# Performance work log

Hardware: AMD Instinct MI355X
Metric: run time of the kernel (lower is better)

Reference implementation:

```python
import jax, jax.numpy as jnp
import numpy as np

NUM_LAYERS = 16
ALPHA = 1.0
EPS = 1e-20

def setup_inputs() -> dict:
    key = jax.random.key(0)
    k1, k2, k3, k4 = jax.random.split(key, 4)
    B, S, M, G = 8, 9, 8, 512
    M2 = M * M
    return {
        "dict_real": jax.random.normal(k1, (B, S, M2, G), dtype=jnp.float32),
        "dict_imag": jax.random.normal(k2, (B, S, M2, G), dtype=jnp.float32),
        "cov_real": jax.random.normal(k3, (B, S, M, M), dtype=jnp.float32),
        "cov_imag": jax.random.normal(k4, (B, S, M, M), dtype=jnp.float32),
    }

def reference(dict_real, dict_imag, cov_real, cov_imag):
    D = (dict_real + 1j * dict_imag).astype(jnp.complex64)   # (B,S,M2,G) dictionary_band
    C = (cov_real + 1j * cov_imag).astype(jnp.complex64)     # (B,S,M,M) covariance matrix
    B, S, M, _ = C.shape
    G = D.shape[-1]
    # covariance_vector = cov.transpose(2,3).reshape(B,S,M2,1)
    r = jnp.swapaxes(C, 2, 3).reshape(B, S, M * M, 1)
    Dh = jnp.conj(jnp.swapaxes(D, 2, 3))                     # (B,S,G,M2)
    DhD = jnp.matmul(Dh, D)                                  # (B,S,G,G) Hermitian PSD
    Dhr = jnp.matmul(Dh, r)                                  # (B,S,G,1)
    # initial spectrum: real part, L2-normalized over grid dim
    res = jnp.real(Dhr).astype(jnp.float32)
    res = res / (jnp.linalg.norm(res, axis=2, keepdims=True) + EPS)
    # gamma = 1 / max|eig(D^H D)|; Hermitian PSD so eigvalsh gives same max magnitude
    eig = jnp.linalg.eigvalsh(DhD)                           # (B,S,G) real
    gamma = 1.0 / jnp.max(jnp.abs(eig), axis=2, keepdims=True)        # (B,S,1)
    lam = 0.5 * jnp.max(jnp.abs(Dhr), axis=2, keepdims=True).reshape(B, S, 1)
    theta = (ALPHA * lam * gamma).reshape(B, S, 1, 1)
    g = gamma.reshape(B, S, 1, 1).astype(jnp.complex64)
    I = jnp.eye(G, dtype=jnp.complex64)
    Wt = I - g * DhD                                         # (B,S,G,G)
    Wer = g * Dhr                                            # We @ r, constant per layer

    def step(res_c, _):
        s = jnp.matmul(Wt, res_c.astype(jnp.complex64)) + Wer
        res_new = jax.nn.relu(jnp.abs(s) - theta)            # soft-shrinkage on magnitude
        return res_new, res_new

    res_final, res_all = jax.lax.scan(step, res, None, length=NUM_LAYERS)
    result_init_all = jnp.moveaxis(res_all, 0, 2)            # (B,S,L,G,1)

    def minmax_norm(x):
        lo = jnp.min(x, axis=2, keepdims=True)
        hi = jnp.max(x, axis=2, keepdims=True)
        return (x - lo) / (hi - lo + EPS)

    result_ave = minmax_norm(jnp.mean(res_final, axis=1, keepdims=True).astype(jnp.float32))
    result = minmax_norm(res_final)
    return (result, result_ave, result_init_all)
```

## Files before the change

### kernel.cpp

```cpp
#include <hip/hip_runtime.h>
#include <math.h>

#define N_SQ   7
#define INV_P  (1.0f / 256.0f)
#define EPS_F  1e-20f
#define PH     72
#define PQ     67

typedef _Float16 h2    __attribute__((ext_vector_type(2)));
typedef _Float16 f16x8 __attribute__((ext_vector_type(8)));
typedef float    f32x4 __attribute__((ext_vector_type(4)));

__device__ inline float cdot2(h2 a, h2 b, float c) {
#if __has_builtin(__builtin_amdgcn_fdot2)
    return __builtin_amdgcn_fdot2(a, b, c, false);
#else
    return c + (float)a.x * (float)b.x + (float)a.y * (float)b.y;
#endif
}
__device__ inline h2 bch2(unsigned int x) { return __builtin_bit_cast(h2, x); }
__device__ inline h2 bch2f(float x)       { return __builtin_bit_cast(h2, x); }
__device__ inline float bcf(h2 x)         { return __builtin_bit_cast(float, x); }


__global__ __launch_bounds__(512, 1) void ista_main_kernel(
    const float* __restrict__ Dre, const float* __restrict__ Dim,
    const float* __restrict__ Cre, const float* __restrict__ Cim,
    float* __restrict__ out, float* __restrict__ ws)
{
    const int bs = blockIdx.x;
    const int t  = threadIdx.x;
    const int wv = t >> 6;
    const int ln = t & 63;
    const int c16 = ln & 15;
    const int qd  = ln >> 4;
    const float* __restrict__ dre = Dre + (size_t)bs * 32768;
    const float* __restrict__ dim = Dim + (size_t)bs * 32768;

    __shared__ __align__(16) float uBuf[9216];
    _Float16* ShRe = (_Float16*)uBuf;
    _Float16* ShIm = (_Float16*)uBuf + 64 * PH;
    float*    Q1   = uBuf + 4608;
    float*    sUp  = uBuf;
    float*    sHu  = uBuf + 1024;
    _Float16* sResH = (_Float16*)(uBuf + 1152);
    __shared__ __align__(16) float s_r[128];
    __shared__ float s_red[16];
    __shared__ float s_scal[8];

    if (t < 64) {
        int i = t >> 3, j = t & 7;
        s_r[2 * t]     = Cre[bs * 64 + j * 8 + i];
        s_r[2 * t + 1] = Cim[bs * 64 + j * 8 + i];
    }
    __syncthreads();

    float dhr_re = 0.f, dhr_im = 0.f;
    h2 dV[64];
    #pragma unroll
    for (int m = 0; m < 64; ++m) {
        float ar = dre[m * 512 + t], ai = dim[m * 512 + t];
        dV[m] = h2{(_Float16)ar, (_Float16)ai};
        float rr = s_r[2 * m], ri = s_r[2 * m + 1];
        dhr_re += ar * rr + ai * ri;
        dhr_im += ar * ri - ai * rr;
    }
    {
        float sv = dhr_re * dhr_re;
        float mv = sqrtf(dhr_re * dhr_re + dhr_im * dhr_im);
        for (int off = 32; off; off >>= 1) {
            sv += __shfl_down(sv, off, 64);
            mv = fmaxf(mv, __shfl_down(mv, off, 64));
        }
        if (ln == 0) { s_red[wv] = sv; s_red[8 + wv] = mv; }
        __syncthreads();
        if (t == 0) {
            float ss = 0.f, mm = 0.f;
            for (int k = 0; k < 8; ++k) { ss += s_red[k]; mm = fmaxf(mm, s_red[8 + k]); }
            s_scal[7] = ss; s_scal[2] = mm;
        }
        __syncthreads();
    }
    float res_g = dhr_re / (sqrtf(s_scal[7]) + EPS_F);

    const int tau0 = 2 * wv, tau1 = 2 * wv + 1;
    const int I0 = tau0 >> 2, J0 = tau0 & 3;
    const int I1 = tau1 >> 2, J1 = tau1 & 3;

    auto epilogue = [&](f32x4 P0, f32x4 Qa0, f32x4 P1, f32x4 Qa1, bool first, bool last) {
        #pragma unroll
        for (int r = 0; r < 4; ++r) {
            Q1[(I0 * 16 + qd * 4 + r) * PQ + J0 * 16 + c16] = Qa0[r];
            Q1[(I1 * 16 + qd * 4 + r) * PQ + J1 * 16 + c16] = Qa1[r];
        }
        float dv = 0.f;
        if (I0 == J0) {
            #pragma unroll
            for (int r = 0; r < 4; ++r) if (qd * 4 + r == c16) dv = fmaxf(dv, fabsf(P0[r]));
        }
        if (I1 == J1) {
            #pragma unroll
            for (int r = 0; r < 4; ++r) if (qd * 4 + r == c16) dv = fmaxf(dv, fabsf(P1[r]));
        }
        for (int off = 32; off; off >>= 1) dv = fmaxf(dv, __shfl_down(dv, off, 64));
        if (ln == 0) s_red[wv] = dv;
        __syncthreads();
        if (t == 0) {
            float m = 0.f;
            for (int k = 0; k < 8; ++k) m = fmaxf(m, s_red[k]);
            s_scal[3] = first ? logf(m) : 2.f * s_scal[3] + logf(m);
            s_scal[4] = 1.f / m;
        }
        __syncthreads();
        float ic = s_scal[4];
        float ci0[4], ci1[4];
        #pragma unroll
        for (int r = 0; r < 4; ++r) {
            ci0[r] = Qa0[r] - Q1[(J0 * 16 + c16) * PQ + I0 * 16 + qd * 4 + r];
            ci1[r] = Qa1[r] - Q1[(J1 * 16 + c16) * PQ + I1 * 16 + qd * 4 + r];
        }
        if (!last) {
            #pragma unroll
            for (int r = 0; r < 4; ++r) {
                ShRe[(I0 * 16 + qd * 4 + r) * PH + J0 * 16 + c16] = (_Float16)(P0[r] * ic);
                ShIm[(I0 * 16 + qd * 4 + r) * PH + J0 * 16 + c16] = (_Float16)(ci0[r] * ic);
                ShRe[(I1 * 16 + qd * 4 + r) * PH + J1 * 16 + c16] = (_Float16)(P1[r] * ic);
                ShIm[(I1 * 16 + qd * 4 + r) * PH + J1 * 16 + c16] = (_Float16)(ci1[r] * ic);
            }
            __syncthreads();
        } else {
            float fr = 0.f;
            #pragma unroll
            for (int r = 0; r < 4; ++r)
                fr += P0[r] * P0[r] + ci0[r] * ci0[r] + P1[r] * P1[r] + ci1[r] * ci1[r];
            fr *= ic * ic;
            for (int off = 32; off; off >>= 1) fr += __shfl_down(fr, off, 64);
            if (ln == 0) s_red[wv] = fr;
            __syncthreads();
            if (t == 0) {
                float fsum = 0.f;
                for (int k = 0; k < 8; ++k) fsum += s_red[k];
                float loglam = (2.f * s_scal[3] + logf(fsum)) * INV_P;
                float gamma = expf(-loglam);
                s_scal[0] = gamma;
                s_scal[1] = 0.5f * s_scal[2] * gamma;
            }
            __syncthreads();
        }
    };

    h2 du_re[32], du_im[32];
    f32x4 gP0 = {0.f, 0.f, 0.f, 0.f}, gQ0 = {0.f, 0.f, 0.f, 0.f};
    f32x4 gP1 = {0.f, 0.f, 0.f, 0.f}, gQ1 = {0.f, 0.f, 0.f, 0.f};
    {
        const int srow = t >> 4;
        const int scb  = (t & 15) * 4;
        float4 pr0, pi0, pr1, pi1;
        pr0 = *(const float4*)&dre[srow * 512 + scb];
        pi0 = *(const float4*)&dim[srow * 512 + scb];
        pr1 = *(const float4*)&dre[(srow + 32) * 512 + scb];
        pi1 = *(const float4*)&dim[(srow + 32) * 512 + scb];
        for (int ch = 0; ch < 8; ++ch) {
            *(h2*)&ShRe[srow * PH + scb]     = h2{(_Float16)pr0.x, (_Float16)pr0.y};
            *(h2*)&ShRe[srow * PH + scb + 2] = h2{(_Float16)pr0.z, (_Float16)pr0.w};
            *(h2*)&ShIm[srow * PH + scb]     = h2{(_Float16)pi0.x, (_Float16)pi0.y};
            *(h2*)&ShIm[srow * PH + scb + 2] = h2{(_Float16)pi0.z, (_Float16)pi0.w};
            *(h2*)&ShRe[(srow + 32) * PH + scb]     = h2{(_Float16)pr1.x, (_Float16)pr1.y};
            *(h2*)&ShRe[(srow + 32) * PH + scb + 2] = h2{(_Float16)pr1.z, (_Float16)pr1.w};
            *(h2*)&ShIm[(srow + 32) * PH + scb]     = h2{(_Float16)pi1.x, (_Float16)pi1.y};
            *(h2*)&ShIm[(srow + 32) * PH + scb + 2] = h2{(_Float16)pi1.z, (_Float16)pi1.w};
            if (ch < 7) {
                int gc = (ch + 1) * 64;
                pr0 = *(const float4*)&dre[srow * 512 + gc + scb];
                pi0 = *(const float4*)&dim[srow * 512 + gc + scb];
                pr1 = *(const float4*)&dre[(srow + 32) * 512 + gc + scb];
                pi1 = *(const float4*)&dim[(srow + 32) * 512 + gc + scb];
            }
            __syncthreads();
            #pragma unroll
            for (int ks = 0; ks < 64; ks += 32) {
                f16x8 arI0 = *(const f16x8*)&ShRe[(I0 * 16 + c16) * PH + ks + qd * 8];
                f16x8 aiI0 = *(const f16x8*)&ShIm[(I0 * 16 + c16) * PH + ks + qd * 8];
                f16x8 arJ0 = *(const f16x8*)&ShRe[(J0 * 16 + c16) * PH + ks + qd * 8];
                f16x8 aiJ0 = *(const f16x8*)&ShIm[(J0 * 16 + c16) * PH + ks + qd * 8];
                gP0 = __builtin_amdgcn_mfma_f32_16x16x32_f16(arI0, arJ0, gP0, 0, 0, 0);
                gP0 = __builtin_amdgcn_mfma_f32_16x16x32_f16(aiI0, aiJ0, gP0, 0, 0, 0);
                gQ0 = __builtin_amdgcn_mfma_f32_16x16x32_f16(aiI0, arJ0, gQ0, 0, 0, 0);
                f16x8 arI1 = *(const f16x8*)&ShRe[(I1 * 16 + c16) * PH + ks + qd * 8];
                f16x8 aiI1 = *(const f16x8*)&ShIm[(I1 * 16 + c16) * PH + ks + qd * 8];
                f16x8 arJ1 = *(const f16x8*)&ShRe[(J1 * 16 + c16) * PH + ks + qd * 8];
                f16x8 aiJ1 = *(const f16x8*)&ShIm[(J1 * 16 + c16) * PH + ks + qd * 8];
                gP1 = __builtin_amdgcn_mfma_f32_16x16x32_f16(arI1, arJ1, gP1, 0, 0, 0);
                gP1 = __builtin_amdgcn_mfma_f32_16x16x32_f16(aiI1, aiJ1, gP1, 0, 0, 0);
                gQ1 = __builtin_amdgcn_mfma_f32_16x16x32_f16(aiI1, arJ1, gQ1, 0, 0, 0);
            }
            if (ch == wv) {
                #pragma unroll
                for (int c = 0; c < 8; ++c) {
                    uint4 aw = *(const uint4*)&ShRe[ln * PH + 8 * c];
                    du_re[4 * c + 0] = bch2(aw.x); du_re[4 * c + 1] = bch2(aw.y);
                    du_re[4 * c + 2] = bch2(aw.z); du_re[4 * c + 3] = bch2(aw.w);
                    uint4 bw = *(const uint4*)&ShIm[ln * PH + 8 * c];
                    du_im[4 * c + 0] = bch2(bw.x); du_im[4 * c + 1] = bch2(bw.y);
                    du_im[4 * c + 2] = bch2(bw.z); du_im[4 * c + 3] = bch2(bw.w);
                }
            }
            __syncthreads();
        }
    }
    epilogue(gP0, gQ0, gP1, gQ1, true, false);

    for (int sq = 0; sq < N_SQ; ++sq) {
        f32x4 P0 = {0.f, 0.f, 0.f, 0.f}, Qa0 = {0.f, 0.f, 0.f, 0.f};
        f32x4 P1 = {0.f, 0.f, 0.f, 0.f}, Qa1 = {0.f, 0.f, 0.f, 0.f};
        #pragma unroll
        for (int ks = 0; ks < 64; ks += 32) {
            f16x8 arI0 = *(const f16x8*)&ShRe[(I0 * 16 + c16) * PH + ks + qd * 8];
            f16x8 aiI0 = *(const f16x8*)&ShIm[(I0 * 16 + c16) * PH + ks + qd * 8];
            f16x8 arJ0 = *(const f16x8*)&ShRe[(J0 * 16 + c16) * PH + ks + qd * 8];
            f16x8 aiJ0 = *(const f16x8*)&ShIm[(J0 * 16 + c16) * PH + ks + qd * 8];
            P0  = __builtin_amdgcn_mfma_f32_16x16x32_f16(arI0, arJ0, P0, 0, 0, 0);
            P0  = __builtin_amdgcn_mfma_f32_16x16x32_f16(aiI0, aiJ0, P0, 0, 0, 0);
            Qa0 = __builtin_amdgcn_mfma_f32_16x16x32_f16(aiI0, arJ0, Qa0, 0, 0, 0);
            f16x8 arI1 = *(const f16x8*)&ShRe[(I1 * 16 + c16) * PH + ks + qd * 8];
            f16x8 aiI1 = *(const f16x8*)&ShIm[(I1 * 16 + c16) * PH + ks + qd * 8];
            f16x8 arJ1 = *(const f16x8*)&ShRe[(J1 * 16 + c16) * PH + ks + qd * 8];
            f16x8 aiJ1 = *(const f16x8*)&ShIm[(J1 * 16 + c16) * PH + ks + qd * 8];
            P1  = __builtin_amdgcn_mfma_f32_16x16x32_f16(arI1, arJ1, P1, 0, 0, 0);
            P1  = __builtin_amdgcn_mfma_f32_16x16x32_f16(aiI1, aiJ1, P1, 0, 0, 0);
            Qa1 = __builtin_amdgcn_mfma_f32_16x16x32_f16(aiI1, arJ1, Qa1, 0, 0, 0);
        }
        epilogue(P0, Qa0, P1, Qa1, false, sq == N_SQ - 1);
    }

    const float gamma = s_scal[0];
    const float theta = s_scal[1];
    float* out_init = out + 40960 + (size_t)bs * 8192;
    const int resh_base = 64 * wv;

    for (int l = 0; l < 16; ++l) {
        sResH[t] = (_Float16)res_g;
        float upR = 0.f, upI = 0.f;
        #pragma unroll
        for (int c = 0; c < 8; ++c) {
            uint4 rw = *(const uint4*)&sResH[resh_base + 8 * c];
            h2 r0 = bch2(rw.x), r1 = bch2(rw.y), r2 = bch2(rw.z), r3 = bch2(rw.w);
            upR = cdot2(du_re[4 * c + 0], r0, upR);  upI = cdot2(du_im[4 * c + 0], r0, upI);
            upR = cdot2(du_re[4 * c + 1], r1, upR);  upI = cdot2(du_im[4 * c + 1], r1, upI);
            upR = cdot2(du_re[4 * c + 2], r2, upR);  upI = cdot2(du_im[4 * c + 2], r2, upI);
            upR = cdot2(du_re[4 * c + 3], r3, upR);  upI = cdot2(du_im[4 * c + 3], r3, upI);
        }
        *(float2*)&sUp[(wv * 64 + ln) * 2] = make_float2(upR, upI);
        __syncthreads();
        if (wv == 0) {
            float ufR = 0.f, ufI = 0.f;
            #pragma unroll
            for (int w8 = 0; w8 < 8; ++w8) {
                float2 p = *(const float2*)&sUp[(w8 * 64 + ln) * 2];
                ufR += p.x; ufI += p.y;
            }
            h2 hu1 = h2{(_Float16)ufR, (_Float16)ufI};
            h2 hu2 = h2{(_Float16)ufI, (_Float16)(-ufR)};
            *(float2*)&sHu[2 * ln] = make_float2(bcf(hu1), bcf(hu2));
        }
        __syncthreads();
        float wR = 0.f, wI = 0.f;
        #pragma unroll
        for (int mm = 0; mm < 32; ++mm) {
            float4 hq = *(const float4*)&sHu[4 * mm];
            wR = cdot2(dV[2 * mm],     bch2f(hq.x), wR);
            wI = cdot2(dV[2 * mm],     bch2f(hq.y), wI);
            wR = cdot2(dV[2 * mm + 1], bch2f(hq.z), wR);
            wI = cdot2(dV[2 * mm + 1], bch2f(hq.w), wI);
        }
        float sre = res_g + gamma * (dhr_re - wR);
        float sim = gamma * (dhr_im - wI);
        float mag = sqrtf(sre * sre + sim * sim);
        res_g = fmaxf(mag - theta, 0.f);
        out_init[l * 512 + t] = res_g;
    }

    {
        float mn = res_g, mx = res_g;
        for (int off = 32; off; off >>= 1) {
            mn = fminf(mn, __shfl_down(mn, off, 64));
            mx = fmaxf(mx, __shfl_down(mx, off, 64));
        }
        if (ln == 0) { s_red[wv] = mn; s_red[8 + wv] = mx; }
        __syncthreads();
        if (t == 0) {
            float a = s_red[0], b2 = s_red[8];
            for (int k = 1; k < 8; ++k) { a = fminf(a, s_red[k]); b2 = fmaxf(b2, s_red[8 + k]); }
            s_scal[5] = a; s_scal[6] = b2;
        }
        __syncthreads();
        out[bs * 512 + t] = (res_g - s_scal[5]) / (s_scal[6] - s_scal[5] + EPS_F);
        ws[bs * 512 + t] = res_g;
    }
}

__global__ __launch_bounds__(512) void ista_ave_kernel(
    const float* __restrict__ ws, float* __restrict__ out)
{
    const int b = blockIdx.x;
    const int g = threadIdx.x;
    __shared__ float s_red[16];
    __shared__ float s_scal[2];
    float acc = 0.f;
    #pragma unroll
    for (int s = 0; s < 9; ++s) acc += ws[(b * 9 + s) * 512 + g];
    acc *= (1.f / 9.f);
    float mn = acc, mx = acc;
    for (int off = 32; off; off >>= 1) {
        mn = fminf(mn, __shfl_down(mn, off, 64));
        mx = fmaxf(mx, __shfl_down(mx, off, 64));
    }
    if ((g & 63) == 0) { s_red[g >> 6] = mn; s_red[8 + (g >> 6)] = mx; }
    __syncthreads();
    if (g == 0) {
        float a = s_red[0], b2 = s_red[8];
        for (int k = 1; k < 8; ++k) { a = fminf(a, s_red[k]); b2 = fmaxf(b2, s_red[8 + k]); }
        s_scal[0] = a; s_scal[1] = b2;
    }
    __syncthreads();
    out[36864 + b * 512 + g] = (acc - s_scal[0]) / (s_scal[1] - s_scal[0] + EPS_F);
}

extern "C" void kernel_launch(void* const* d_in, const int* in_sizes, int n_in,
                              void* d_out, int out_size, void* d_ws, size_t ws_size,
                              hipStream_t stream) {
    const float* Dre = (const float*)d_in[0];
    const float* Dim = (const float*)d_in[1];
    const float* Cre = (const float*)d_in[2];
    const float* Cim = (const float*)d_in[3];
    float* out = (float*)d_out;
    float* ws  = (float*)d_ws;

    ista_main_kernel<<<72, 512, 0, stream>>>(Dre, Dim, Cre, Cim, out, ws);
    ista_ave_kernel<<<8, 512, 0, stream>>>(ws, out);
}
```

Before: 112.6 us.

## Double-buffer Gram staging, replace thread-0 reductions with redundant all-thread reductions, shuffle-broadcast updates

The Gram-matrix staging loop now alternates between two LDS buffers, which drops one barrier per chunk, and it folds the dictionary register loads and the D^H r accumulation into that same loop. Scalar reductions that thread 0 used to do through shared memory are now done redundantly by every thread, removing extra barriers. In the ISTA layers, the separate wave-0 reduction and its second barrier are replaced by every wave reducing the partial sums and broadcasting them with wave shuffles. Dual accumulators shorten the dependency chains, and launch bounds are raised to two blocks per CU, which may force register spills given the large per-thread register arrays.

```diff
diff --git a/kernel.cpp b/kernel.cpp
--- a/kernel.cpp
+++ b/kernel.cpp
@@ -23,7 +23,7 @@
 __device__ inline float bcf(h2 x)         { return __builtin_bit_cast(float, x); }
 
 
-__global__ __launch_bounds__(512, 1) void ista_main_kernel(
+__global__ __launch_bounds__(512, 2) void ista_main_kernel(
     const float* __restrict__ Dre, const float* __restrict__ Dim,
     const float* __restrict__ Cre, const float* __restrict__ Cim,
     float* __restrict__ out, float* __restrict__ ws)
@@ -38,33 +38,161 @@
     const float* __restrict__ dim = Dim + (size_t)bs * 32768;
 
     __shared__ __align__(16) float uBuf[9216];
-    _Float16* ShRe = (_Float16*)uBuf;
-    _Float16* ShIm = (_Float16*)uBuf + 64 * PH;
-    float*    Q1   = uBuf + 4608;
-    float*    sUp  = uBuf;
-    float*    sHu  = uBuf + 1024;
-    _Float16* sResH = (_Float16*)(uBuf + 1152);
+    _Float16* ShRe  = (_Float16*)uBuf;
+    _Float16* ShIm  = (_Float16*)uBuf + 64 * PH;
+    _Float16* ShReB = (_Float16*)uBuf + 2 * 64 * PH;
+    _Float16* ShImB = (_Float16*)uBuf + 3 * 64 * PH;
+    float*    Q1    = uBuf + 4608;
+    _Float16* sResH = (_Float16*)(uBuf + 2048);
     __shared__ __align__(16) float s_r[128];
     __shared__ float s_red[16];
-    __shared__ float s_scal[8];
 
     if (t < 64) {
         int i = t >> 3, j = t & 7;
         s_r[2 * t]     = Cre[bs * 64 + j * 8 + i];
         s_r[2 * t + 1] = Cim[bs * 64 + j * 8 + i];
     }
-    __syncthreads();
-
-    float dhr_re = 0.f, dhr_im = 0.f;
+
+    const int tau0 = 2 * wv, tau1 = 2 * wv + 1;
+    const int I0 = tau0 >> 2, J0 = tau0 & 3;
+    const int I1 = tau1 >> 2, J1 = tau1 & 3;
+
+    float Elog = 0.f, gamma = 0.f, theta = 0.f, mm = 0.f;
+
+    auto epilogue = [&](f32x4 P0, f32x4 Qa0, f32x4 P1, f32x4 Qa1, bool first, bool last) {
+        #pragma unroll
+        for (int r = 0; r < 4; ++r) {
+            Q1[(I0 * 16 + qd * 4 + r) * PQ + J0 * 16 + c16] = Qa0[r];
+            Q1[(I1 * 16 + qd * 4 + r) * PQ + J1 * 16 + c16] = Qa1[r];
+        }
+        float dv = 0.f;
+        if (I0 == J0) {
+            #pragma unroll
+            for (int r = 0; r < 4; ++r) if (qd * 4 + r == c16) dv = fmaxf(dv, fabsf(P0[r]));
+        }
+        if (I1 == J1) {
+            #pragma unroll
+            for (int r = 0; r < 4; ++r) if (qd * 4 + r == c16) dv = fmaxf(dv, fabsf(P1[r]));
+        }
+        for (int off = 32; off; off >>= 1) dv = fmaxf(dv, __shfl_down(dv, off, 64));
+        if (ln == 0) s_red[wv] = dv;
+        __syncthreads();
+        float m = s_red[0];
+        #pragma unroll
+        for (int k = 1; k < 8; ++k) m = fmaxf(m, s_red[k]);
+        Elog = first ? logf(m) : 2.f * Elog + logf(m);
+        float ic = 1.f / m;
+        float ci0[4], ci1[4];
+        #pragma unroll
+        for (int r = 0; r < 4; ++r) {
+            ci0[r] = Qa0[r] - Q1[(J0 * 16 + c16) * PQ + I0 * 16 + qd * 4 + r];
+            ci1[r] = Qa1[r] - Q1[(J1 * 16 + c16) * PQ + I1 * 16 + qd * 4 + r];
+        }
+        if (!last) {
+            #pragma unroll
+            for (int r = 0; r < 4; ++r) {
+                ShRe[(I0 * 16 + qd * 4 + r) * PH + J0 * 16 + c16] = (_Float16)(P0[r] * ic);
+                ShIm[(I0 * 16 + qd * 4 + r) * PH + J0 * 16 + c16] = (_Float16)(ci0[r] * ic);
+                ShRe[(I1 * 16 + qd * 4 + r) * PH + J1 * 16 + c16] = (_Float16)(P1[r] * ic);
+                ShIm[(I1 * 16 + qd * 4 + r) * PH + J1 * 16 + c16] = (_Float16)(ci1[r] * ic);
+            }
+            __syncthreads();
+        } else {
+            float fr = 0.f;
+            #pragma unroll
+            for (int r = 0; r < 4; ++r)
+                fr += P0[r] * P0[r] + ci0[r] * ci0[r] + P1[r] * P1[r] + ci1[r] * ci1[r];
+            fr *= ic * ic;
+            for (int off = 32; off; off >>= 1) fr += __shfl_down(fr, off, 64);
+            if (ln == 0) s_red[8 + wv] = fr;
+            __syncthreads();
+            float fsum = 0.f;
+            #pragma unroll
+            for (int k = 0; k < 8; ++k) fsum += s_red[8 + k];
+            float loglam = (2.f * Elog + logf(fsum)) * INV_P;
+            gamma = expf(-loglam);
+            theta = 0.5f * mm * gamma;
+        }
+    };
+
     h2 dV[64];
-    #pragma unroll
-    for (int m = 0; m < 64; ++m) {
-        float ar = dre[m * 512 + t], ai = dim[m * 512 + t];
-        dV[m] = h2{(_Float16)ar, (_Float16)ai};
-        float rr = s_r[2 * m], ri = s_r[2 * m + 1];
-        dhr_re += ar * rr + ai * ri;
-        dhr_im += ar * ri - ai * rr;
-    }
+    h2 du_re[32], du_im[32];
+    float dr0 = 0.f, dr1 = 0.f, di0 = 0.f, di1 = 0.f;
+    f32x4 gP0 = {0.f,0.f,0.f,0.f}, gQ0 = {0.f,0.f,0.f,0.f};
+    f32x4 gP1 = {0.f,0.f,0.f,0.f}, gQ1 = {0.f,0.f,0.f,0.f};
+    {
+        const int srow = t >> 4;
+        const int scb  = (t & 15) * 4;
+        float4 pr0 = *(const float4*)&dre[srow * 512 + scb];
+        float4 pi0 = *(const float4*)&dim[srow * 512 + scb];
+        float4 pr1 = *(const float4*)&dre[(srow + 32) * 512 + scb];
+        float4 pi1 = *(const float4*)&dim[(srow + 32) * 512 + scb];
+        #pragma unroll
+        for (int ch = 0; ch < 8; ++ch) {
+            _Float16* SRe = (ch & 1) ? ShReB : ShRe;
+            _Float16* SIm = (ch & 1) ? ShImB : ShIm;
+            *(h2*)&SRe[srow * PH + scb]       = h2{(_Float16)pr0.x, (_Float16)pr0.y};
+            *(h2*)&SRe[srow * PH + scb + 2]   = h2{(_Float16)pr0.z, (_Float16)pr0.w};
+            *(h2*)&SIm[srow * PH + scb]       = h2{(_Float16)pi0.x, (_Float16)pi0.y};
+            *(h2*)&SIm[srow * PH + scb + 2]   = h2{(_Float16)pi0.z, (_Float16)pi0.w};
+            *(h2*)&SRe[(srow + 32) * PH + scb]     = h2{(_Float16)pr1.x, (_Float16)pr1.y};
+            *(h2*)&SRe[(srow + 32) * PH + scb + 2] = h2{(_Float16)pr1.z, (_Float16)pr1.w};
+            *(h2*)&SIm[(srow + 32) * PH + scb]     = h2{(_Float16)pi1.x, (_Float16)pi1.y};
+            *(h2*)&SIm[(srow + 32) * PH + scb + 2] = h2{(_Float16)pi1.z, (_Float16)pi1.w};
+            if (ch < 7) {
+                int gc = (ch + 1) * 64;
+                pr0 = *(const float4*)&dre[srow * 512 + gc + scb];
+                pi0 = *(const float4*)&dim[srow * 512 + gc + scb];
+                pr1 = *(const float4*)&dre[(srow + 32) * 512 + gc + scb];
+                pi1 = *(const float4*)&dim[(srow + 32) * 512 + gc + scb];
+            }
+            float cr[8], cim8[8];
+            #pragma unroll
+            for (int k = 0; k < 8; ++k) {
+                cr[k]   = dre[(ch * 8 + k) * 512 + t];
+                cim8[k] = dim[(ch * 8 + k) * 512 + t];
+            }
+            __syncthreads();
+            #pragma unroll
+            for (int ks = 0; ks < 64; ks += 32) {
+                f16x8 arI0 = *(const f16x8*)&SRe[(I0 * 16 + c16) * PH + ks + qd * 8];
+                f16x8 aiI0 = *(const f16x8*)&SIm[(I0 * 16 + c16) * PH + ks + qd * 8];
+                f16x8 arJ0 = *(const f16x8*)&SRe[(J0 * 16 + c16) * PH + ks + qd * 8];
+                f16x8 aiJ0 = *(const f16x8*)&SIm[(J0 * 16 + c16) * PH + ks + qd * 8];
+                gP0 = __builtin_amdgcn_mfma_f32_16x16x32_f16(arI0, arJ0, gP0, 0, 0, 0);
+                gP0 = __builtin_amdgcn_mfma_f32_16x16x32_f16(aiI0, aiJ0, gP0, 0, 0, 0);
+                gQ0 = __builtin_amdgcn_mfma_f32_16x16x32_f16(aiI0, arJ0, gQ0, 0, 0, 0);
+                f16x8 arI1 = *(const f16x8*)&SRe[(I1 * 16 + c16) * PH + ks + qd * 8];
+                f16x8 aiI1 = *(const f16x8*)&SIm[(I1 * 16 + c16) * PH + ks + qd * 8];
+                f16x8 arJ1 = *(const f16x8*)&SRe[(J1 * 16 + c16) * PH + ks + qd * 8];
+                f16x8 aiJ1 = *(const f16x8*)&SIm[(J1 * 16 + c16) * PH + ks + qd * 8];
+                gP1 = __builtin_amdgcn_mfma_f32_16x16x32_f16(arI1, arJ1, gP1, 0, 0, 0);
+                gP1 = __builtin_amdgcn_mfma_f32_16x16x32_f16(aiI1, aiJ1, gP1, 0, 0, 0);
+                gQ1 = __builtin_amdgcn_mfma_f32_16x16x32_f16(aiI1, arJ1, gQ1, 0, 0, 0);
+            }
+            if (ch == wv) {
+                #pragma unroll
+                for (int c = 0; c < 8; ++c) {
+                    uint4 aw = *(const uint4*)&SRe[ln * PH + 8 * c];
+                    du_re[4 * c + 0] = bch2(aw.x); du_re[4 * c + 1] = bch2(aw.y);
+                    du_re[4 * c + 2] = bch2(aw.z); du_re[4 * c + 3] = bch2(aw.w);
+                    uint4 bw = *(const uint4*)&SIm[ln * PH + 8 * c];
+                    du_im[4 * c + 0] = bch2(bw.x); du_im[4 * c + 1] = bch2(bw.y);
+                    du_im[4 * c + 2] = bch2(bw.z); du_im[4 * c + 3] = bch2(bw.w);
+                }
+            }
+            #pragma unroll
+            for (int k = 0; k < 8; ++k) {
+                float ar = cr[k], ai = cim8[k];
+                dV[ch * 8 + k] = h2{(_Float16)ar, (_Float16)ai};
+                float rr = s_r[2 * (ch * 8 + k)], ri = s_r[2 * (ch * 8 + k) + 1];
+                if (k & 1) { dr1 += ar * rr + ai * ri; di1 += ar * ri - ai * rr; }
+                else       { dr0 += ar * rr + ai * ri; di0 += ar * ri - ai * rr; }
+            }
+        }
+    }
+    const float dhr_re = dr0 + dr1, dhr_im = di0 + di1;
+    float res_g;
     {
         float sv = dhr_re * dhr_re;
         float mv = sqrtf(dhr_re * dhr_re + dhr_im * dhr_im);
@@ -74,145 +202,18 @@
         }
         if (ln == 0) { s_red[wv] = sv; s_red[8 + wv] = mv; }
         __syncthreads();
-        if (t == 0) {
-            float ss = 0.f, mm = 0.f;
-            for (int k = 0; k < 8; ++k) { ss += s_red[k]; mm = fmaxf(mm, s_red[8 + k]); }
-            s_scal[7] = ss; s_scal[2] = mm;
-        }
-        __syncthreads();
-    }
-    float res_g = dhr_re / (sqrtf(s_scal[7]) + EPS_F);
-
-    const int tau0 = 2 * wv, tau1 = 2 * wv + 1;
-    const int I0 = tau0 >> 2, J0 = tau0 & 3;
-    const int I1 = tau1 >> 2, J1 = tau1 & 3;
-
-    auto epilogue = [&](f32x4 P0, f32x4 Qa0, f32x4 P1, f32x4 Qa1, bool first, bool last) {
-        #pragma unroll
-        for (int r = 0; r < 4; ++r) {
-            Q1[(I0 * 16 + qd * 4 + r) * PQ + J0 * 16 + c16] = Qa0[r];
-            Q1[(I1 * 16 + qd * 4 + r) * PQ + J1 * 16 + c16] = Qa1[r];
-        }
-        float dv = 0.f;
-        if (I0 == J0) {
-            #pragma unroll
-            for (int r = 0; r < 4; ++r) if (qd * 4 + r == c16) dv = fmaxf(dv, fabsf(P0[r]));
-        }
-        if (I1 == J1) {
-            #pragma unroll
-            for (int r = 0; r < 4; ++r) if (qd * 4 + r == c16) dv = fmaxf(dv, fabsf(P1[r]));
-        }
-        for (int off = 32; off; off >>= 1) dv = fmaxf(dv, __shfl_down(dv, off, 64));
-        if (ln == 0) s_red[wv] = dv;
-        __syncthreads();
-        if (t == 0) {
-            float m = 0.f;
-            for (int k = 0; k < 8; ++k) m = fmaxf(m, s_red[k]);
-            s_scal[3] = first ? logf(m) : 2.f * s_scal[3] + logf(m);
-            s_scal[4] = 1.f / m;
-        }
-        __syncthreads();
-        float ic = s_scal[4];
-        float ci0[4], ci1[4];
-        #pragma unroll
-        for (int r = 0; r < 4; ++r) {
-            ci0[r] = Qa0[r] - Q1[(J0 * 16 + c16) * PQ + I0 * 16 + qd * 4 + r];
-            ci1[r] = Qa1[r] - Q1[(J1 * 16 + c16) * PQ + I1 * 16 + qd * 4 + r];
-        }
-        if (!last) {
-            #pragma unroll
-            for (int r = 0; r < 4; ++r) {
-                ShRe[(I0 * 16 + qd * 4 + r) * PH + J0 * 16 + c16] = (_Float16)(P0[r] * ic);
-                ShIm[(I0 * 16 + qd * 4 + r) * PH + J0 * 16 + c16] = (_Float16)(ci0[r] * ic);
-                ShRe[(I1 * 16 + qd * 4 + r) * PH + J1 * 16 + c16] = (_Float16)(P1[r] * ic);
-                ShIm[(I1 * 16 + qd * 4 + r) * PH + J1 * 16 + c16] = (_Float16)(ci1[r] * ic);
-            }
-            __syncthreads();
-        } else {
-            float fr = 0.f;
-            #pragma unroll
-            for (int r = 0; r < 4; ++r)
-                fr += P0[r] * P0[r] + ci0[r] * ci0[r] + P1[r] * P1[r] + ci1[r] * ci1[r];
-            fr *= ic * ic;
-            for (int off = 32; off; off >>= 1) fr += __shfl_down(fr, off, 64);
-            if (ln == 0) s_red[wv] = fr;
-            __syncthreads();
-            if (t == 0) {
-                float fsum = 0.f;
-                for (int k = 0; k < 8; ++k) fsum += s_red[k];
-                float loglam = (2.f * s_scal[3] + logf(fsum)) * INV_P;
-                float gamma = expf(-loglam);
-                s_scal[0] = gamma;
-                s_scal[1] = 0.5f * s_scal[2] * gamma;
-            }
-            __syncthreads();
-        }
-    };
-
-    h2 du_re[32], du_im[32];
-    f32x4 gP0 = {0.f, 0.f, 0.f, 0.f}, gQ0 = {0.f, 0.f, 0.f, 0.f};
-    f32x4 gP1 = {0.f, 0.f, 0.f, 0.f}, gQ1 = {0.f, 0.f, 0.f, 0.f};
-    {
-        const int srow = t >> 4;
-        const int scb  = (t & 15) * 4;
-        float4 pr0, pi0, pr1, pi1;
-        pr0 = *(const float4*)&dre[srow * 512 + scb];
-        pi0 = *(const float4*)&dim[srow * 512 + scb];
-        pr1 = *(const float4*)&dre[(srow + 32) * 512 + scb];
-        pi1 = *(const float4*)&dim[(srow + 32) * 512 + scb];
-        for (int ch = 0; ch < 8; ++ch) {
-            *(h2*)&ShRe[srow * PH + scb]     = h2{(_Float16)pr0.x, (_Float16)pr0.y};
-            *(h2*)&ShRe[srow * PH + scb + 2] = h2{(_Float16)pr0.z, (_Float16)pr0.w};
-            *(h2*)&ShIm[srow * PH + scb]     = h2{(_Float16)pi0.x, (_Float16)pi0.y};
-            *(h2*)&ShIm[srow * PH + scb + 2] = h2{(_Float16)pi0.z, (_Float16)pi0.w};
-            *(h2*)&ShRe[(srow + 32) * PH + scb]     = h2{(_Float16)pr1.x, (_Float16)pr1.y};
-            *(h2*)&ShRe[(srow + 32) * PH + scb + 2] = h2{(_Float16)pr1.z, (_Float16)pr1.w};
-            *(h2*)&ShIm[(srow + 32) * PH + scb]     = h2{(_Float16)pi1.x, (_Float16)pi1.y};
-            *(h2*)&ShIm[(srow + 32) * PH + scb + 2] = h2{(_Float16)pi1.z, (_Float16)pi1.w};
-            if (ch < 7) {
-                int gc = (ch + 1) * 64;
-                pr0 = *(const float4*)&dre[srow * 512 + gc + scb];
-                pi0 = *(const float4*)&dim[srow * 512 + gc + scb];
-                pr1 = *(const float4*)&dre[(srow + 32) * 512 + gc + scb];
-                pi1 = *(const float4*)&dim[(srow + 32) * 512 + gc + scb];
-            }
-            __syncthreads();
-            #pragma unroll
-            for (int ks = 0; ks < 64; ks += 32) {
-                f16x8 arI0 = *(const f16x8*)&ShRe[(I0 * 16 + c16) * PH + ks + qd * 8];
-                f16x8 aiI0 = *(const f16x8*)&ShIm[(I0 * 16 + c16) * PH + ks + qd * 8];
-                f16x8 arJ0 = *(const f16x8*)&ShRe[(J0 * 16 + c16) * PH + ks + qd * 8];
-                f16x8 aiJ0 = *(const f16x8*)&ShIm[(J0 * 16 + c16) * PH + ks + qd * 8];
-                gP0 = __builtin_amdgcn_mfma_f32_16x16x32_f16(arI0, arJ0, gP0, 0, 0, 0);
-                gP0 = __builtin_amdgcn_mfma_f32_16x16x32_f16(aiI0, aiJ0, gP0, 0, 0, 0);
-                gQ0 = __builtin_amdgcn_mfma_f32_16x16x32_f16(aiI0, arJ0, gQ0, 0, 0, 0);
-                f16x8 arI1 = *(const f16x8*)&ShRe[(I1 * 16 + c16) * PH + ks + qd * 8];
-                f16x8 aiI1 = *(const f16x8*)&ShIm[(I1 * 16 + c16) * PH + ks + qd * 8];
-                f16x8 arJ1 = *(const f16x8*)&ShRe[(J1 * 16 + c16) * PH + ks + qd * 8];
-                f16x8 aiJ1 = *(const f16x8*)&ShIm[(J1 * 16 + c16) * PH + ks + qd * 8];
-                gP1 = __builtin_amdgcn_mfma_f32_16x16x32_f16(arI1, arJ1, gP1, 0, 0, 0);
-                gP1 = __builtin_amdgcn_mfma_f32_16x16x32_f16(aiI1, aiJ1, gP1, 0, 0, 0);
-                gQ1 = __builtin_amdgcn_mfma_f32_16x16x32_f16(aiI1, arJ1, gQ1, 0, 0, 0);
-            }
-            if (ch == wv) {
-                #pragma unroll
-                for (int c = 0; c < 8; ++c) {
-                    uint4 aw = *(const uint4*)&ShRe[ln * PH + 8 * c];
-                    du_re[4 * c + 0] = bch2(aw.x); du_re[4 * c + 1] = bch2(aw.y);
-                    du_re[4 * c + 2] = bch2(aw.z); du_re[4 * c + 3] = bch2(aw.w);
-                    uint4 bw = *(const uint4*)&ShIm[ln * PH + 8 * c];
-                    du_im[4 * c + 0] = bch2(bw.x); du_im[4 * c + 1] = bch2(bw.y);
-                    du_im[4 * c + 2] = bch2(bw.z); du_im[4 * c + 3] = bch2(bw.w);
-                }
-            }
-            __syncthreads();
-        }
+        float ss = 0.f; mm = 0.f;
+        #pragma unroll
+        for (int k = 0; k < 8; ++k) { ss += s_red[k]; mm = fmaxf(mm, s_red[8 + k]); }
+        res_g = dhr_re / (sqrtf(ss) + EPS_F);
+        __syncthreads();
     }
     epilogue(gP0, gQ0, gP1, gQ1, true, false);
 
+    #pragma unroll 1
     for (int sq = 0; sq < N_SQ; ++sq) {
-        f32x4 P0 = {0.f, 0.f, 0.f, 0.f}, Qa0 = {0.f, 0.f, 0.f, 0.f};
-        f32x4 P1 = {0.f, 0.f, 0.f, 0.f}, Qa1 = {0.f, 0.f, 0.f, 0.f};
+        f32x4 P0 = {0.f,0.f,0.f,0.f}, Qa0 = {0.f,0.f,0.f,0.f};
+        f32x4 P1 = {0.f,0.f,0.f,0.f}, Qa1 = {0.f,0.f,0.f,0.f};
         #pragma unroll
         for (int ks = 0; ks < 64; ks += 32) {
             f16x8 arI0 = *(const f16x8*)&ShRe[(I0 * 16 + c16) * PH + ks + qd * 8];
@@ -233,48 +234,43 @@
         epilogue(P0, Qa0, P1, Qa1, false, sq == N_SQ - 1);
     }
 
-    const float gamma = s_scal[0];
-    const float theta = s_scal[1];
     float* out_init = out + 40960 + (size_t)bs * 8192;
     const int resh_base = 64 * wv;
 
+    #pragma unroll 2
     for (int l = 0; l < 16; ++l) {
         sResH[t] = (_Float16)res_g;
-        float upR = 0.f, upI = 0.f;
+        float upR0 = 0.f, upR1 = 0.f, upI0 = 0.f, upI1 = 0.f;
         #pragma unroll
         for (int c = 0; c < 8; ++c) {
             uint4 rw = *(const uint4*)&sResH[resh_base + 8 * c];
             h2 r0 = bch2(rw.x), r1 = bch2(rw.y), r2 = bch2(rw.z), r3 = bch2(rw.w);
-            upR = cdot2(du_re[4 * c + 0], r0, upR);  upI = cdot2(du_im[4 * c + 0], r0, upI);
-            upR = cdot2(du_re[4 * c + 1], r1, upR);  upI = cdot2(du_im[4 * c + 1], r1, upI);
-            upR = cdot2(du_re[4 * c + 2], r2, upR);  upI = cdot2(du_im[4 * c + 2], r2, upI);
-            upR = cdot2(du_re[4 * c + 3], r3, upR);  upI = cdot2(du_im[4 * c + 3], r3, upI);
-        }
-        *(float2*)&sUp[(wv * 64 + ln) * 2] = make_float2(upR, upI);
-        __syncthreads();
-        if (wv == 0) {
-            float ufR = 0.f, ufI = 0.f;
-            #pragma unroll
-            for (int w8 = 0; w8 < 8; ++w8) {
-                float2 p = *(const float2*)&sUp[(w8 * 64 + ln) * 2];
-                ufR += p.x; ufI += p.y;
-            }
-            h2 hu1 = h2{(_Float16)ufR, (_Float16)ufI};
-            h2 hu2 = h2{(_Float16)ufI, (_Float16)(-ufR)};
-            *(float2*)&sHu[2 * ln] = make_float2(bcf(hu1), bcf(hu2));
-        }
-        __syncthreads();
-        float wR = 0.f, wI = 0.f;
-        #pragma unroll
-        for (int mm = 0; mm < 32; ++mm) {
-            float4 hq = *(const float4*)&sHu[4 * mm];
-            wR = cdot2(dV[2 * mm],     bch2f(hq.x), wR);
-            wI = cdot2(dV[2 * mm],     bch2f(hq.y), wI);
-            wR = cdot2(dV[2 * mm + 1], bch2f(hq.z), wR);
-            wI = cdot2(dV[2 * mm + 1], bch2f(hq.w), wI);
-        }
-        float sre = res_g + gamma * (dhr_re - wR);
-        float sim = gamma * (dhr_im - wI);
+            upR0 = cdot2(du_re[4 * c + 0], r0, upR0);  upI0 = cdot2(du_im[4 * c + 0], r0, upI0);
+            upR1 = cdot2(du_re[4 * c + 1], r1, upR1);  upI1 = cdot2(du_im[4 * c + 1], r1, upI1);
+            upR0 = cdot2(du_re[4 * c + 2], r2, upR0);  upI0 = cdot2(du_im[4 * c + 2], r2, upI0);
+            upR1 = cdot2(du_re[4 * c + 3], r3, upR1);  upI1 = cdot2(du_im[4 * c + 3], r3, upI1);
+        }
+        float* myUp = uBuf + (l & 1) * 1024;
+        *(float2*)&myUp[t * 2] = make_float2(upR0 + upR1, upI0 + upI1);
+        __syncthreads();
+        float uR = 0.f, uI = 0.f;
+        #pragma unroll
+        for (int w8 = 0; w8 < 8; ++w8) {
+            float2 p = *(const float2*)&myUp[(w8 * 64 + ln) * 2];
+            uR += p.x; uI += p.y;
+        }
+        float fa = bcf(h2{(_Float16)uR, (_Float16)uI});
+        float fb = bcf(h2{(_Float16)uI, (_Float16)(-uR)});
+        float wR0 = 0.f, wR1 = 0.f, wI0 = 0.f, wI1 = 0.f;
+        #pragma unroll
+        for (int m2 = 0; m2 < 64; m2 += 2) {
+            float a0 = __shfl(fa, m2, 64),     b0 = __shfl(fb, m2, 64);
+            float a1 = __shfl(fa, m2 + 1, 64), b1 = __shfl(fb, m2 + 1, 64);
+            wR0 = cdot2(dV[m2],     bch2f(a0), wR0);  wI0 = cdot2(dV[m2],     bch2f(b0), wI0);
+            wR1 = cdot2(dV[m2 + 1], bch2f(a1), wR1);  wI1 = cdot2(dV[m2 + 1], bch2f(b1), wI1);
+        }
+        float sre = res_g + gamma * (dhr_re - (wR0 + wR1));
+        float sim = gamma * (dhr_im - (wI0 + wI1));
         float mag = sqrtf(sre * sre + sim * sim);
         res_g = fmaxf(mag - theta, 0.f);
         out_init[l * 512 + t] = res_g;
@@ -288,13 +284,10 @@
         }
         if (ln == 0) { s_red[wv] = mn; s_red[8 + wv] = mx; }
         __syncthreads();
-        if (t == 0) {
-            float a = s_red[0], b2 = s_red[8];
-            for (int k = 1; k < 8; ++k) { a = fminf(a, s_red[k]); b2 = fmaxf(b2, s_red[8 + k]); }
-            s_scal[5] = a; s_scal[6] = b2;
-        }
-        __syncthreads();
-        out[bs * 512 + t] = (res_g - s_scal[5]) / (s_scal[6] - s_scal[5] + EPS_F);
+        float lo = s_red[0], hi = s_red[8];
+        #pragma unroll
+        for (int k = 1; k < 8; ++k) { lo = fminf(lo, s_red[k]); hi = fmaxf(hi, s_red[8 + k]); }
+        out[bs * 512 + t] = (res_g - lo) / (hi - lo + EPS_F);
         ws[bs * 512 + t] = res_g;
     }
 }
@@ -305,7 +298,6 @@
     const int b = blockIdx.x;
     const int g = threadIdx.x;
     __shared__ float s_red[16];
-    __shared__ float s_scal[2];
     float acc = 0.f;
     #pragma unroll
     for (int s = 0; s < 9; ++s) acc += ws[(b * 9 + s) * 512 + g];
@@ -317,13 +309,10 @@
     }
     if ((g & 63) == 0) { s_red[g >> 6] = mn; s_red[8 + (g >> 6)] = mx; }
     __syncthreads();
-    if (g == 0) {
-        float a = s_red[0], b2 = s_red[8];
-        for (int k = 1; k < 8; ++k) { a = fminf(a, s_red[k]); b2 = fmaxf(b2, s_red[8 + k]); }
-        s_scal[0] = a; s_scal[1] = b2;
-    }
-    __syncthreads();
-    out[36864 + b * 512 + g] = (acc - s_scal[0]) / (s_scal[1] - s_scal[0] + EPS_F);
+    float lo = s_red[0], hi = s_red[8];
+    #pragma unroll
+    for (int k = 1; k < 8; ++k) { lo = fminf(lo, s_red[k]); hi = fmaxf(hi, s_red[8 + k]); }
+    out[36864 + b * 512 + g] = (acc - lo) / (hi - lo + EPS_F);
 }
 
 extern "C" void kernel_launch(void* const* d_in, const int* in_sizes, int n_in,
```

Result: slower. 171.6 us (+52.4%).
